# Kernel optimization log

Hardware: AMD Instinct MI355X
Metric: run time of the kernel (lower is better)

The kernel has to match this reference:

```python
import jax, jax.numpy as jnp
import numpy as np

B, N, D = 4, 2048, 2048
HEADS, KV_HEADS = 16, 4
DH = D // HEADS            # 128 per-head dim
KV_RATIO = HEADS // KV_HEADS
MAX_LEN, MAX_BSZ = 2048, 4
EPS = 1.1920929e-07        # torch.finfo(float32).eps (RMSNorm default eps=None)


def _rot_tables(n, d, base=10000.0):
    thetas = base ** (-jnp.arange(0, d, 2, dtype=jnp.float32) / d)   # [d/2]
    ang = jnp.arange(n, dtype=jnp.float32)[:, None] * thetas[None, :]
    cos = jnp.repeat(jnp.cos(ang), 2, axis=-1)   # [n, d] interleaved pairs
    sin = jnp.repeat(jnp.sin(ang), 2, axis=-1)
    return cos, sin


def _rotate_half_inverted(x):
    x1 = x[..., ::2]
    x2 = x[..., 1::2]
    return jnp.stack([-x2, x1], axis=-1).reshape(x.shape)


def _apply_rotation(x, end, start=0):
    cos, sin = _rot_tables(MAX_LEN, DH)
    return x * cos[start:end] + _rotate_half_inverted(x) * sin[start:end]


def setup_inputs() -> dict:
    key = jax.random.key(0)
    ks = jax.random.split(key, 4)
    s = 0.02
    return {
        "x": jax.random.normal(ks[0], (B, N, D), jnp.float32),
        "norm_w": jnp.ones((D,), jnp.float32),
        "qw": jax.random.normal(ks[1], (HEADS * DH, D), jnp.float32) * s,
        "qb": jnp.zeros((HEADS * DH,), jnp.float32),
        "kvw": jax.random.normal(ks[2], (2 * DH * KV_HEADS, D), jnp.float32) * s,
        "kvb": jnp.zeros((2 * DH * KV_HEADS,), jnp.float32),
        "wow": jax.random.normal(ks[3], (D, HEADS * DH), jnp.float32) * s,
        "wob": jnp.zeros((D,), jnp.float32),
        "kv_cache": jnp.zeros((MAX_BSZ, MAX_LEN, 2 * DH * KV_HEADS), jnp.float32),
        "pos": 0,
    }


def reference(x, norm_w, qw, qb, kvw, kvb, wow, wob, kv_cache, pos):
    b, n, d = x.shape
    t = pos + n  # total cached length
    # RMSNorm
    xn = x * jax.lax.rsqrt(jnp.mean(x * x, axis=-1, keepdims=True) + EPS) * norm_w
    # Q projection -> [b, heads, n, dh]
    q = (xn @ qw.T + qb).reshape(b, n, HEADS, DH).transpose(0, 2, 1, 3)
    # KV projection + cache write/read
    kv = xn @ kvw.T + kvb                                  # [b, n, 2*dh*kv_heads]
    cache = jax.lax.dynamic_update_slice(kv_cache, kv, (0, pos, 0))
    kvf = cache[:b, :t].reshape(b, t, KV_HEADS, 2 * DH).transpose(0, 2, 1, 3)
    kvf = jnp.repeat(kvf, KV_RATIO, axis=1)                # GQA expand -> [b, heads, t, 2dh]
    k, v = kvf[..., :DH], kvf[..., DH:]
    # RoPE (interleaved-pair variant)
    q = _apply_rotation(q, t, pos)
    k = _apply_rotation(k, t, 0)
    # Attention (decoder causal)
    attn = jnp.einsum("bhqd,bhkd->bhqk", q, k) / jnp.sqrt(jnp.float32(DH))
    if n > 1:
        mask = jnp.triu(jnp.ones((n, t), bool), k=1 + pos)
        attn = jnp.where(mask, -jnp.inf, attn)
    attn = jax.nn.softmax(attn, axis=-1)
    o = jnp.einsum("bhqk,bhkd->bhqd", attn, v).transpose(0, 2, 1, 3).reshape(b, n, HEADS * DH)
    return o @ wow.T + wob
```

## Files before the change

kernel.cpp:

```cpp
#include <hip/hip_runtime.h>
#include <hip/hip_bf16.h>

typedef unsigned short u16;
typedef unsigned int u32;
typedef __attribute__((ext_vector_type(4))) float f32x4;
typedef __attribute__((ext_vector_type(8))) short s16x8;

#define B_ 4
#define N_ 2048
#define D_ 2048
#define HEADS_ 16
#define KVH_ 4
#define DH_ 128
#define KVD_ 1024
#define M_ 8192
#define QSCALE2_ 0.12753257518622628f

__device__ __forceinline__ u16 f2bf(float f) {
  u32 u = __builtin_bit_cast(u32, f);
  return (u16)((u + 0x7FFFu + ((u >> 16) & 1u)) >> 16);
}

__device__ __forceinline__ float fexp2(float x) {
#if __has_builtin(__builtin_amdgcn_exp2f)
  return __builtin_amdgcn_exp2f(x);
#else
  return exp2f(x);
#endif
}

__device__ __forceinline__ void gload_lds16(const void* g, void* l) {
  __builtin_amdgcn_global_load_lds(
      (const __attribute__((address_space(1))) u32*)g,
      (__attribute__((address_space(3))) u32*)l, 16, 0, 0);
}

__global__ __launch_bounds__(256)
void rope_tab_k(float* __restrict__ cost, float* __restrict__ sint)
{
  const int idx = blockIdx.x * 256 + threadIdx.x;
  const int p = idx >> 6, i = idx & 63;
  const float theta = expf(-(float)i * 0.015625f * 9.210340371976184f);
  float s, c;
  sincosf((float)p * theta, &s, &c);
  cost[idx] = c;
  sint[idx] = s;
}

__global__ __launch_bounds__(256)
void cvt_bf16_k(const float* __restrict__ s, u16* __restrict__ d, int n)
{
  const int i = (blockIdx.x * 256 + threadIdx.x) * 8;
  if (i >= n) return;
  const f32x4 a = *(const f32x4*)(s + i);
  const f32x4 b = *(const f32x4*)(s + i + 4);
  s16x8 o;
  #pragma unroll
  for (int j = 0; j < 4; ++j) { o[j] = (short)f2bf(a[j]); o[4 + j] = (short)f2bf(b[j]); }
  *(s16x8*)(d + i) = o;
}

__global__ __launch_bounds__(256)
void rmsnorm_k(const float* __restrict__ x, const float* __restrict__ w, u16* __restrict__ xn)
{
  const int row = blockIdx.x, t = threadIdx.x;
  const float* xr = x + (size_t)row * D_;
  const f32x4 a = *(const f32x4*)(xr + t * 8);
  const f32x4 b = *(const f32x4*)(xr + t * 8 + 4);
  float ss = a[0]*a[0] + a[1]*a[1] + a[2]*a[2] + a[3]*a[3]
           + b[0]*b[0] + b[1]*b[1] + b[2]*b[2] + b[3]*b[3];
  #pragma unroll
  for (int off = 32; off >= 1; off >>= 1) ss += __shfl_xor(ss, off);
  __shared__ float wss[4];
  if ((t & 63) == 0) wss[t >> 6] = ss;
  __syncthreads();
  const float tot = wss[0] + wss[1] + wss[2] + wss[3];
  const float rs = rsqrtf(tot * (1.0f / D_) + 1.1920929e-07f);
  s16x8 o;
  #pragma unroll
  for (int j = 0; j < 4; ++j) {
    o[j]     = (short)f2bf(a[j] * rs * w[t * 8 + j]);
    o[4 + j] = (short)f2bf(b[j] * rs * w[t * 8 + 4 + j]);
  }
  *(s16x8*)(xn + (size_t)row * D_ + t * 8) = o;
}

template<int EPI>
__global__ __launch_bounds__(512, 2)
void gemm_p(const u16* __restrict__ A, const u16* __restrict__ Bw,
            void* __restrict__ Cv, void* __restrict__ Cv2, u16* __restrict__ Vt,
            const float* __restrict__ bias, const float* __restrict__ bias2,
            const float* __restrict__ cos_t, const float* __restrict__ sin_t)
{
  __shared__ __align__(16) u16 As[2][8192];
  __shared__ __align__(16) u16 Bs[2][4096];
  const int t = threadIdx.x, w = t >> 6, l = t & 63;
  const int g = l >> 4, lr = l & 15;
  const int wm = w >> 2, wn = w & 3;

  const int nbx = gridDim.x;
  const int nb = nbx * gridDim.y;
  const int flat = blockIdx.y * nbx + blockIdx.x;
  const int swz = (flat & 7) * (nb >> 3) + (flat >> 3);
  const int row0 = (swz / nbx) * 256, col0 = (swz % nbx) * 128;

  const int NT = 64;

  const int srow = w * 16 + (l >> 2);
  const int scol = ((((l & 3) - ((l >> 3) & 3)) & 3)) * 8;
  const u16* gA = A + (size_t)(row0 + srow) * 2048 + scol;
  const u16* gB = Bw + (size_t)(col0 + srow) * 2048 + scol;

  const int rc = (g + ((lr >> 1) & 3)) & 3;

  f32x4 acc[8][2] = {};

  auto stage_tile = [&](int kt2, int pb) {
    gload_lds16(gA + (size_t)kt2 * 32, &As[pb][(w * 16) * 32]);
    gload_lds16(gA + (size_t)128 * 2048 + kt2 * 32, &As[pb][(128 + w * 16) * 32]);
    gload_lds16(gB + (size_t)kt2 * 32, &Bs[pb][(w * 16) * 32]);
  };

  stage_tile(0, 0);

  for (int kt = 0; kt < NT; ++kt) {
    const int p = kt & 1;
    if (kt + 1 < NT) {
      stage_tile(kt + 1, p ^ 1);
      asm volatile("s_waitcnt vmcnt(3)" ::: "memory");
    } else {
      asm volatile("s_waitcnt vmcnt(0)" ::: "memory");
    }
    __builtin_amdgcn_s_barrier();

    s16x8 bf[2], af[8];
    #pragma unroll
    for (int nf = 0; nf < 2; ++nf)
      bf[nf] = *(const s16x8*)(&Bs[p][(wn * 32 + nf * 16 + lr) * 32 + rc * 8]);
    #pragma unroll
    for (int mf = 0; mf < 8; ++mf)
      af[mf] = *(const s16x8*)(&As[p][(wm * 128 + mf * 16 + lr) * 32 + rc * 8]);

    __builtin_amdgcn_s_setprio(1);
    #pragma unroll
    for (int mf = 0; mf < 8; ++mf)
      #pragma unroll
      for (int nf = 0; nf < 2; ++nf)
        acc[mf][nf] = __builtin_amdgcn_mfma_f32_16x16x32_bf16(af[mf], bf[nf], acc[mf][nf], 0, 0, 0);
    __builtin_amdgcn_s_setprio(0);
    __builtin_amdgcn_sched_barrier(0);
    __builtin_amdgcn_s_barrier();
  }

  #pragma unroll
  for (int mf = 0; mf < 8; ++mf) {
    #pragma unroll
    for (int nf = 0; nf < 2; ++nf) {
      const int cc = col0 + wn * 32 + nf * 16 + lr;
      const float bv = (EPI == 4 && cc >= 2048) ? bias2[cc - 2048] : bias[cc];
      const int rr0 = row0 + wm * 128 + mf * 16 + g * 4;
      if (EPI == 4 && cc >= 2048 && ((cc - 2048) & 255) >= 128) {
        const int ccc = cc - 2048;
        const int kh2 = ccc >> 8, d = (ccc & 255) - 128;
        u32 lo, hi;
        {
          const u16 p0 = f2bf(acc[mf][nf][0] + bv);
          const u16 p1 = f2bf(acc[mf][nf][1] + bv);
          const u16 p2 = f2bf(acc[mf][nf][2] + bv);
          const u16 p3 = f2bf(acc[mf][nf][3] + bv);
          lo = (u32)p0 | ((u32)p1 << 16);
          hi = (u32)p2 | ((u32)p3 << 16);
        }
        const int bb = rr0 >> 11, pos0 = rr0 & 2047;
        u32* dst = (u32*)(Vt + ((size_t)((bb * KVH_ + kh2) * DH_ + d)) * 2048 + pos0);
        dst[0] = lo;
        dst[1] = hi;
      } else {
        #pragma unroll
        for (int j = 0; j < 4; ++j) {
          const int rr = rr0 + j;
          float v = acc[mf][nf][j] + bv;
          if (EPI == 0) {
            ((float*)Cv)[(size_t)rr * 2048 + cc] = v;
          } else {
            const int pos = rr & (N_ - 1);
            const float pv = __shfl_xor(v, 1);
            if (cc < 2048) {
              const int d = cc & (DH_ - 1);
              const float c = cos_t[pos * 64 + (d >> 1)];
              const float s = sin_t[pos * 64 + (d >> 1)];
              const float o = (cc & 1) ? fmaf(v, c, pv * s) : fmaf(v, c, -pv * s);
              ((u16*)Cv)[(size_t)rr * 2048 + cc] = f2bf(o);
            } else {
              const int ccc = cc - 2048;
              const int dm = ccc & 255;
              const float c = cos_t[pos * 64 + (dm >> 1)];
              const float s = sin_t[pos * 64 + (dm >> 1)];
              const float o = (dm & 1) ? fmaf(v, c, pv * s) : fmaf(v, c, -pv * s);
              ((u16*)Cv2)[(size_t)rr * 1024 + ccc] = f2bf(o);
            }
          }
        }
      }
    }
  }
}

__global__ __launch_bounds__(512, 1)
void attn_k(const u16* __restrict__ q, const u16* __restrict__ kvb,
            const u16* __restrict__ vt, u16* __restrict__ out)
{
  const int fi = blockIdx.x, h = blockIdx.y, b = blockIdx.z;
  const int kh = h >> 2;
  const int t = threadIdx.x, w = t >> 6, lane = t & 63;
  const int g = lane >> 4, lr = lane & 15;

  __shared__ __align__(16) u16 Ks[2][64 * 128];
  __shared__ __align__(16) u16 Vs[2][128 * 64];
  __shared__ __align__(16) u16 Ps[8][32 * 64];

  const int kc = 2 * w;
  const int kr0 = kc * 4 + (lane >> 4);
  const int ksw0 = (lane & 15) ^ (kr0 & 7);
  const int kr1 = kr0 + 4;
  const int ksw1 = (lane & 15) ^ (kr1 & 7);
  const int vd0 = kc * 8 + (lane >> 3);
  const int vsw0 = (lane & 7) ^ (vd0 & 7);
  const int vd1 = vd0 + 8;
  const int vsw1 = (lane & 7) ^ (vd1 & 7);

  const u16* kbase = kvb + (size_t)b * (N_ * KVD_) + kh * 256;
  const u16* vbase = vt + (size_t)((b * KVH_ + kh) * DH_) * N_;

  int cur = 0;

  auto issue = [&](int kt, int buf) {
    gload_lds16(kbase + (size_t)(kt * 64 + kr0) * KVD_ + ksw0 * 8, &Ks[buf][kc * 512]);
    gload_lds16(kbase + (size_t)(kt * 64 + kr1) * KVD_ + ksw1 * 8, &Ks[buf][(kc + 1) * 512]);
    gload_lds16(vbase + (size_t)vd0 * N_ + kt * 64 + vsw0 * 8, &Vs[buf][kc * 512]);
    gload_lds16(vbase + (size_t)vd1 * N_ + kt * 64 + vsw1 * 8, &Vs[buf][(kc + 1) * 512]);
  };

  auto run_qtile = [&](int qi, int nkt, bool chain) {
    const int qrow0 = qi * 256 + w * 32;
    const int td = (qrow0 + 31) >> 6;
    s16x8 qf[2][4];
    #pragma unroll
    for (int r = 0; r < 2; ++r) {
      const u16* qp = q + (size_t)(b * N_ + qrow0 + r * 16 + lr) * D_ + h * DH_;
      #pragma unroll
      for (int ks = 0; ks < 4; ++ks) qf[r][ks] = *(const s16x8*)(qp + ks * 32 + g * 8);
    }
    f32x4 o_acc[2][8] = {};
    float m_j[2][4], l_j[2][4];
    #pragma unroll
    for (int r = 0; r < 2; ++r)
      #pragma unroll
      for (int j = 0; j < 4; ++j) { m_j[r][j] = -1e30f; l_j[r][j] = 0.0f; }

    for (int kt = 0; kt < nkt; ++kt) {
      __syncthreads();
      if (kt + 1 < nkt)      issue(kt + 1, cur ^ 1);
      else if (chain)        issue(0, cur ^ 1);

      if (kt <= td) {
        const u16* Kc = &Ks[cur][0];
        const u16* Vc = &Vs[cur][0];

        f32x4 sf[2][4] = {};
        __builtin_amdgcn_s_setprio(1);
        #pragma unroll
        for (int ks = 0; ks < 4; ++ks) {
          #pragma unroll
          for (int kvf = 0; kvf < 4; ++kvf) {
            const int kvr = kvf * 16 + lr;
            const int ba = (kvr * 256 + ks * 64 + g * 16) ^ ((kvr & 7) << 4);
            const s16x8 kf = *(const s16x8*)((const char*)Kc + ba);
            sf[0][kvf] = __builtin_amdgcn_mfma_f32_16x16x32_bf16(qf[0][ks], kf, sf[0][kvf], 0, 0, 0);
            sf[1][kvf] = __builtin_amdgcn_mfma_f32_16x16x32_bf16(qf[1][ks], kf, sf[1][kvf], 0, 0, 0);
          }
        }
        __builtin_amdgcn_s_setprio(0);

        const bool need_mask = (kt == td);
        float pmax[2][4];
        #pragma unroll
        for (int r = 0; r < 2; ++r) {
          #pragma unroll
          for (int j = 0; j < 4; ++j) {
            float mx = -1e30f;
            #pragma unroll
            for (int kvf = 0; kvf < 4; ++kvf) {
              float sv = sf[r][kvf][j] * QSCALE2_;
              if (need_mask) {
                const int kj = kt * 64 + kvf * 16 + lr;
                const int qi_row = qrow0 + r * 16 + g * 4 + j;
                if (kj > qi_row) sv = -1e30f;
              }
              sf[r][kvf][j] = sv;
              mx = fmaxf(mx, sv);
            }
            mx = fmaxf(mx, __shfl_xor(mx, 1));
            mx = fmaxf(mx, __shfl_xor(mx, 2));
            mx = fmaxf(mx, __shfl_xor(mx, 4));
            mx = fmaxf(mx, __shfl_xor(mx, 8));
            pmax[r][j] = mx;
          }
        }

        float needv = -1e30f;
        #pragma unroll
        for (int r = 0; r < 2; ++r)
          #pragma unroll
          for (int j = 0; j < 4; ++j) needv = fmaxf(needv, pmax[r][j] - m_j[r][j]);
        if (__any(needv > 8.0f)) {
          #pragma unroll
          for (int r = 0; r < 2; ++r)
            #pragma unroll
            for (int j = 0; j < 4; ++j) {
              const float mn = fmaxf(m_j[r][j], pmax[r][j]);
              const float pf = fexp2(m_j[r][j] - mn);
              m_j[r][j] = mn;
              l_j[r][j] *= pf;
              #pragma unroll
              for (int df = 0; df < 8; ++df) o_acc[r][df][j] *= pf;
            }
        }

        #pragma unroll
        for (int r = 0; r < 2; ++r) {
          #pragma unroll
          for (int j = 0; j < 4; ++j) {
            float lacc = 0.0f;
            #pragma unroll
            for (int kvf = 0; kvf < 4; ++kvf) {
              const float p = fexp2(sf[r][kvf][j] - m_j[r][j]);
              lacc += p;
              const int rq = r * 16 + g * 4 + j, ck = kvf * 16 + lr;
              const int ba = (rq * 128 + ck * 2) ^ ((rq & 7) << 4);
              *(u16*)((char*)&Ps[w][0] + ba) = (u16)(__builtin_bit_cast(u32, p) >> 16);
            }
            l_j[r][j] += lacc;
          }
        }

        __builtin_amdgcn_s_setprio(1);
        #pragma unroll
        for (int kk = 0; kk < 2; ++kk) {
          s16x8 pf[2];
          #pragma unroll
          for (int r = 0; r < 2; ++r) {
            const int prow = r * 16 + lr;
            const int bap = (prow * 128 + kk * 64 + g * 16) ^ ((prow & 7) << 4);
            pf[r] = *(const s16x8*)((const char*)&Ps[w][0] + bap);
          }
          #pragma unroll
          for (int df = 0; df < 8; ++df) {
            const int dd = df * 16 + lr;
            const int bav = (dd * 128 + kk * 64 + g * 16) ^ ((dd & 7) << 4);
            const s16x8 vf = *(const s16x8*)((const char*)Vc + bav);
            o_acc[0][df] = __builtin_amdgcn_mfma_f32_16x16x32_bf16(pf[0], vf, o_acc[0][df], 0, 0, 0);
            o_acc[1][df] = __builtin_amdgcn_mfma_f32_16x16x32_bf16(pf[1], vf, o_acc[1][df], 0, 0, 0);
          }
        }
        __builtin_amdgcn_s_setprio(0);
      }
      cur ^= 1;
    }

    #pragma unroll
    for (int r = 0; r < 2; ++r) {
      float inv_l[4];
      #pragma unroll
      for (int j = 0; j < 4; ++j) {
        float s4 = l_j[r][j];
        s4 += __shfl_xor(s4, 1);
        s4 += __shfl_xor(s4, 2);
        s4 += __shfl_xor(s4, 4);
        s4 += __shfl_xor(s4, 8);
        inv_l[j] = 1.0f / s4;
      }
      u16* op = out + (size_t)(b * N_ + qrow0 + r * 16) * D_ + h * DH_;
      #pragma unroll
      for (int df = 0; df < 8; ++df)
        #pragma unroll
        for (int j = 0; j < 4; ++j)
          op[(size_t)(g * 4 + j) * D_ + df * 16 + lr] = f2bf(o_acc[r][df][j] * inv_l[j]);
    }
  };

  const int qlo = fi, qhi = 7 - fi;
  issue(0, 0);
  run_qtile(qlo, 4 * qlo + 4, true);
  run_qtile(qhi, 4 * qhi + 4, false);
}

extern "C" void kernel_launch(void* const* d_in, const int* in_sizes, int n_in,
                              void* d_out, int out_size, void* d_ws, size_t ws_size,
                              hipStream_t stream) {
  const float* x      = (const float*)d_in[0];
  const float* normw  = (const float*)d_in[1];
  const float* qw     = (const float*)d_in[2];
  const float* qbias  = (const float*)d_in[3];
  const float* kvw    = (const float*)d_in[4];
  const float* kvbias = (const float*)d_in[5];
  const float* wow    = (const float*)d_in[6];
  const float* wob    = (const float*)d_in[7];
  float* out = (float*)d_out;

  char* ws = (char*)d_ws;
  u16* xn    = (u16*)(ws + 0);
  u16* dq    = (u16*)(ws + 33554432);
  u16* dkv   = (u16*)(ws + 67108864);
  u16* dvt   = (u16*)(ws + 83886080);
  u16* wqkv  = (u16*)(ws + 92274688);
  u16* wowb  = (u16*)(ws + 104857600);
  float* cost = (float*)(ws + 113246208);
  float* sint = (float*)(ws + 113770496);

  rope_tab_k<<<512, 256, 0, stream>>>(cost, sint);
  cvt_bf16_k<<<2048, 256, 0, stream>>>(qw, wqkv, 2048 * 2048);
  cvt_bf16_k<<<1024, 256, 0, stream>>>(kvw, wqkv + 2048 * 2048, 1024 * 2048);
  cvt_bf16_k<<<2048, 256, 0, stream>>>(wow, wowb, 2048 * 2048);
  rmsnorm_k<<<8192, 256, 0, stream>>>(x, normw, xn);
  gemm_p<4><<<dim3(24, 32), 512, 0, stream>>>(xn, wqkv, (void*)dq, (void*)dkv, dvt,
                                              qbias, kvbias, cost, sint);
  attn_k<<<dim3(4, 16, 4), 512, 0, stream>>>(dq, dkv, dvt, xn);
  gemm_p<0><<<dim3(16, 32), 512, 0, stream>>>(xn, wowb, (void*)out, nullptr, nullptr,
                                              wob, nullptr, nullptr, nullptr);
}
```

Baseline: 397.8 us.

## Add dedicated 256x256-tile output GEMM with 4-stage LDS pipeline

Replaces the generic gemm_p<0> used for the output projection with a new gemm_deep kernel. It uses 256x256 tiles, with each wave computing 8x4 MFMA fragments, and a four-buffer global-to-LDS prefetch with explicit vmcnt waits. The aim is more operand reuse per LDS load and deeper latency hiding. The cost is fewer blocks (256) on the GPU and heavier register use. gemm_p's EPI==0 path is removed, so it is now specialised to the QKV epilogue only.

```diff
diff --git a/kernel.cpp b/kernel.cpp
--- a/kernel.cpp
+++ b/kernel.cpp
@@ -157,9 +157,9 @@
     #pragma unroll
     for (int nf = 0; nf < 2; ++nf) {
       const int cc = col0 + wn * 32 + nf * 16 + lr;
-      const float bv = (EPI == 4 && cc >= 2048) ? bias2[cc - 2048] : bias[cc];
+      const float bv = (cc >= 2048) ? bias2[cc - 2048] : bias[cc];
       const int rr0 = row0 + wm * 128 + mf * 16 + g * 4;
-      if (EPI == 4 && cc >= 2048 && ((cc - 2048) & 255) >= 128) {
+      if (cc >= 2048 && ((cc - 2048) & 255) >= 128) {
         const int ccc = cc - 2048;
         const int kh2 = ccc >> 8, d = (ccc & 255) - 128;
         u32 lo, hi;
@@ -180,27 +180,109 @@
         for (int j = 0; j < 4; ++j) {
           const int rr = rr0 + j;
           float v = acc[mf][nf][j] + bv;
-          if (EPI == 0) {
-            ((float*)Cv)[(size_t)rr * 2048 + cc] = v;
+          const int pos = rr & (N_ - 1);
+          const float pv = __shfl_xor(v, 1);
+          if (cc < 2048) {
+            const int d = cc & (DH_ - 1);
+            const float c = cos_t[pos * 64 + (d >> 1)];
+            const float s = sin_t[pos * 64 + (d >> 1)];
+            const float o = (cc & 1) ? fmaf(v, c, pv * s) : fmaf(v, c, -pv * s);
+            ((u16*)Cv)[(size_t)rr * 2048 + cc] = f2bf(o);
           } else {
-            const int pos = rr & (N_ - 1);
-            const float pv = __shfl_xor(v, 1);
-            if (cc < 2048) {
-              const int d = cc & (DH_ - 1);
-              const float c = cos_t[pos * 64 + (d >> 1)];
-              const float s = sin_t[pos * 64 + (d >> 1)];
-              const float o = (cc & 1) ? fmaf(v, c, pv * s) : fmaf(v, c, -pv * s);
-              ((u16*)Cv)[(size_t)rr * 2048 + cc] = f2bf(o);
-            } else {
-              const int ccc = cc - 2048;
-              const int dm = ccc & 255;
-              const float c = cos_t[pos * 64 + (dm >> 1)];
-              const float s = sin_t[pos * 64 + (dm >> 1)];
-              const float o = (dm & 1) ? fmaf(v, c, pv * s) : fmaf(v, c, -pv * s);
-              ((u16*)Cv2)[(size_t)rr * 1024 + ccc] = f2bf(o);
-            }
+            const int ccc = cc - 2048;
+            const int dm = ccc & 255;
+            const float c = cos_t[pos * 64 + (dm >> 1)];
+            const float s = sin_t[pos * 64 + (dm >> 1)];
+            const float o = (dm & 1) ? fmaf(v, c, pv * s) : fmaf(v, c, -pv * s);
+            ((u16*)Cv2)[(size_t)rr * 1024 + ccc] = f2bf(o);
           }
         }
+      }
+    }
+  }
+}
+
+__global__ __launch_bounds__(512, 1)
+void gemm_deep(const u16* __restrict__ A, const u16* __restrict__ Bw,
+               float* __restrict__ Cv, const float* __restrict__ bias)
+{
+  __shared__ __align__(16) u16 As[4][8192];
+  __shared__ __align__(16) u16 Bs[4][8192];
+  const int t = threadIdx.x, w = t >> 6, l = t & 63;
+  const int g = l >> 4, lr = l & 15;
+  const int wm = w >> 2, wn = w & 3;
+
+  const int nbx = gridDim.x;
+  const int nb = nbx * gridDim.y;
+  const int flat = blockIdx.y * nbx + blockIdx.x;
+  const int swz = (flat & 7) * (nb >> 3) + (flat >> 3);
+  const int row0 = (swz / nbx) * 256, col0 = (swz % nbx) * 256;
+
+  const int NT = 64;
+
+  const int srow = w * 16 + (l >> 2);
+  const int scol = ((((l & 3) - ((l >> 3) & 3)) & 3)) * 8;
+  const u16* gA = A + (size_t)(row0 + srow) * 2048 + scol;
+  const u16* gB = Bw + (size_t)(col0 + srow) * 2048 + scol;
+
+  const int rc = (g + ((lr >> 1) & 3)) & 3;
+
+  f32x4 acc[8][4] = {};
+
+  auto stage_tile = [&](int kt2, int pb) {
+    gload_lds16(gA + (size_t)kt2 * 32, &As[pb][(w * 16) * 32]);
+    gload_lds16(gA + (size_t)128 * 2048 + kt2 * 32, &As[pb][(128 + w * 16) * 32]);
+    gload_lds16(gB + (size_t)kt2 * 32, &Bs[pb][(w * 16) * 32]);
+    gload_lds16(gB + (size_t)128 * 2048 + kt2 * 32, &Bs[pb][(128 + w * 16) * 32]);
+  };
+
+  stage_tile(0, 0);
+  stage_tile(1, 1);
+  stage_tile(2, 2);
+
+  for (int kt = 0; kt < NT; ++kt) {
+    const int p = kt & 3;
+    if (kt + 3 < NT) {
+      stage_tile(kt + 3, (kt + 3) & 3);
+      asm volatile("s_waitcnt vmcnt(12)" ::: "memory");
+    } else if (kt + 2 < NT) {
+      asm volatile("s_waitcnt vmcnt(8)" ::: "memory");
+    } else if (kt + 1 < NT) {
+      asm volatile("s_waitcnt vmcnt(4)" ::: "memory");
+    } else {
+      asm volatile("s_waitcnt vmcnt(0)" ::: "memory");
+    }
+    __builtin_amdgcn_s_barrier();
+
+    s16x8 bf[4], af[8];
+    #pragma unroll
+    for (int nf = 0; nf < 4; ++nf)
+      bf[nf] = *(const s16x8*)(&Bs[p][(wn * 64 + nf * 16 + lr) * 32 + rc * 8]);
+    #pragma unroll
+    for (int mf = 0; mf < 8; ++mf)
+      af[mf] = *(const s16x8*)(&As[p][(wm * 128 + mf * 16 + lr) * 32 + rc * 8]);
+
+    __builtin_amdgcn_s_setprio(1);
+    #pragma unroll
+    for (int mf = 0; mf < 8; ++mf)
+      #pragma unroll
+      for (int nf = 0; nf < 4; ++nf)
+        acc[mf][nf] = __builtin_amdgcn_mfma_f32_16x16x32_bf16(af[mf], bf[nf], acc[mf][nf], 0, 0, 0);
+    __builtin_amdgcn_s_setprio(0);
+    __builtin_amdgcn_sched_barrier(0);
+    __builtin_amdgcn_s_barrier();
+  }
+
+  #pragma unroll
+  for (int mf = 0; mf < 8; ++mf) {
+    #pragma unroll
+    for (int nf = 0; nf < 4; ++nf) {
+      const int cc = col0 + wn * 64 + nf * 16 + lr;
+      const float bv = bias[cc];
+      #pragma unroll
+      for (int j = 0; j < 4; ++j) {
+        const int rr = row0 + wm * 128 + mf * 16 + g * 4 + j;
+        Cv[(size_t)rr * 2048 + cc] = acc[mf][nf][j] + bv;
       }
     }
   }
@@ -426,6 +508,5 @@
   gemm_p<4><<<dim3(24, 32), 512, 0, stream>>>(xn, wqkv, (void*)dq, (void*)dkv, dvt,
                                               qbias, kvbias, cost, sint);
   attn_k<<<dim3(4, 16, 4), 512, 0, stream>>>(dq, dkv, dvt, xn);
-  gemm_p<0><<<dim3(16, 32), 512, 0, stream>>>(xn, wowb, (void*)out, nullptr, nullptr,
-                                              wob, nullptr, nullptr, nullptr);
-}
+  gemm_deep<<<dim3(8, 32), 512, 0, stream>>>(xn, wowb, out, wob);
+}
```

New measurement: 408.2 us. 1.03x slower.
